# Performance work log

Measured on AMD Instinct MI355X. Metric: run time of the kernel, lower is better.

## Reference

```python
import jax, jax.numpy as jnp
import numpy as np

L, B, S, D, H, DQ, DH = 6, 2, 1024, 1024, 16, 64, 4096  # layers, batch, seq, d_e, heads, d_q, d_h
EPS = 1e-5


def _ln(x, g, b):
    m = jnp.mean(x, axis=-1, keepdims=True)
    v = jnp.mean(jnp.square(x - m), axis=-1, keepdims=True)
    return (x - m) / jnp.sqrt(v + EPS) * g + b


def setup_inputs() -> dict:
    key = jax.random.key(0)
    ks = jax.random.split(key, 8)
    f = lambda k, shape: (jax.random.normal(k, shape, jnp.float32) * 0.02)
    return {
        "x": jax.random.normal(ks[0], (B, S, D), jnp.float32),
        "mask": jnp.zeros((B, S, S), dtype=bool),
        "Wq": f(ks[1], (L, D, H * DQ)), "bq": jnp.zeros((L, H * DQ), jnp.float32),
        "Wk": f(ks[2], (L, D, H * DQ)), "bk": jnp.zeros((L, H * DQ), jnp.float32),
        "Wv": f(ks[3], (L, D, H * DQ)), "bv": jnp.zeros((L, H * DQ), jnp.float32),
        "Wo": f(ks[4], (L, H * DQ, D)), "bo": jnp.zeros((L, D), jnp.float32),
        "ln1_g": jnp.ones((L, D), jnp.float32), "ln1_b": jnp.zeros((L, D), jnp.float32),
        "W1": f(ks[5], (L, D, DH)), "b1": jnp.zeros((L, DH), jnp.float32),
        "W2": f(ks[6], (L, DH, D)), "b2": jnp.zeros((L, D), jnp.float32),
        "ln2_g": jnp.ones((L, D), jnp.float32), "ln2_b": jnp.zeros((L, D), jnp.float32),
    }


def _encoder(x, mask, Wq, bq, Wk, bk, Wv, bv, Wo, bo, ln1_g, ln1_b, W1, b1, W2, b2, ln2_g, ln2_b):
    scale = 1.0 / np.sqrt(DQ).astype(np.float32)

    def step(h, p):
        wq, q_b, wk, k_b, wv, v_b, wo, o_b, g1, be1, w1, f_b1, w2, f_b2, g2, be2 = p
        q = (h @ wq + q_b).reshape(B, S, H, DQ)
        k = (h @ wk + k_b).reshape(B, S, H, DQ)
        v = (h @ wv + v_b).reshape(B, S, H, DQ)
        scores = jnp.einsum('bqhd,bkhd->bhqk', q, k) * scale  # [B,H,S,S]
        scores = jnp.where(mask[:, None, :, :], jnp.float32(-1e9), scores)
        attn = jax.nn.softmax(scores, axis=-1)
        ctx = jnp.einsum('bhqk,bkhd->bqhd', attn, v).reshape(B, S, H * DQ)
        h = _ln(h + ctx @ wo + o_b, g1, be1)
        ff = jax.nn.relu(h @ w1 + f_b1) @ w2 + f_b2  # 1x1 conv1d FFN == pointwise MLP
        h = _ln(h + ff, g2, be2)
        return h, None

    params = (Wq, bq, Wk, bk, Wv, bv, Wo, bo, ln1_g, ln1_b, W1, b1, W2, b2, ln2_g, ln2_b)
    out, _ = jax.lax.scan(step, x, params)
    return out


def reference(x, mask, Wq, bq, Wk, bk, Wv, bv, Wo, bo, ln1_g, ln1_b, W1, b1, W2, b2, ln2_g, ln2_b):
    return _encoder(x, mask, Wq, bq, Wk, bk, Wv, bv, Wo, bo, ln1_g, ln1_b, W1, b1, W2, b2, ln2_g, ln2_b)
```

## Files before the change

### kernel.cpp

```cpp
#include <hip/hip_runtime.h>


typedef unsigned short u16;
typedef __attribute__((ext_vector_type(8))) short bh8;
typedef __attribute__((ext_vector_type(4))) float f32x4;

#define PLANE (2048ull * 1024ull)

__device__ __forceinline__ u16 f2b(float f) {
    unsigned u = __float_as_uint(f);
    u += 0x7fffu + ((u >> 16) & 1u);
    return (u16)(u >> 16);
}
__device__ __forceinline__ void gl_lds16(const void* g, void* l) {
    __builtin_amdgcn_global_load_lds((const __attribute__((address_space(1))) void*)g,
                                     (__attribute__((address_space(3))) void*)l, 16, 0, 0);
}

#define MFMA(a, b, c) __builtin_amdgcn_mfma_f32_16x16x32_bf16((a), (b), (c), 0, 0, 0)

__device__ __forceinline__ void xcd_remap(int nx, int& bx, int& by) {
    int id = blockIdx.y * nx + blockIdx.x;
    int cpx = (nx * gridDim.y) >> 3;
    int sid = (id & 7) * cpx + (id >> 3);
    bx = sid & (nx - 1);
    by = sid / nx;
}

__global__ __launch_bounds__(256) void init_h(const float* __restrict__ x,
                                              u16* __restrict__ hbf, float* __restrict__ hf, int n4) {
    int i = blockIdx.x * 256 + threadIdx.x;
    if (i < n4) {
        float4 v = ((const float4*)x)[i];
        ((float4*)hf)[i] = v;
        u16 t[4] = { f2b(v.x), f2b(v.y), f2b(v.z), f2b(v.w) };
        ((ushort4*)hbf)[i] = *(const ushort4*)t;
    }
}

__device__ __forceinline__ void tp_tile_f2b(const float* __restrict__ in, u16* __restrict__ out,
                                            int R, int C, int ty, int tx) {
    const int r0 = ty * 64, c0 = tx * 64;
    __shared__ alignas(16) float tile[64][68];
    const int tid = threadIdx.x;
#pragma unroll
    for (int it = 0; it < 4; ++it) {
        int s = it * 256 + tid;
        int rr = s >> 4, c4 = (s & 15) * 4;
        float4 v = *(const float4*)&in[(size_t)(r0 + rr) * C + c0 + c4];
        int gsw = ((c4 >> 2) ^ (rr >> 3)) << 2;
        *(float4*)&tile[rr][gsw] = v;
    }
    __syncthreads();
#pragma unroll
    for (int it = 0; it < 2; ++it) {
        int chunk = it * 256 + tid, cc = chunk >> 3, r8 = chunk & 7;
        u16 tmp[8];
#pragma unroll
        for (int j = 0; j < 8; ++j) {
            int r = r8 * 8 + j;
            int col = ((((cc >> 2) ^ (r >> 3)) << 2) | (cc & 3));
            tmp[j] = f2b(tile[r][col]);
        }
        *(uint4*)&out[(size_t)(c0 + cc) * R + r0 + r8 * 8] = *(const uint4*)tmp;
    }
}

__global__ __launch_bounds__(256) void transpose_weights(
        const float* __restrict__ Wq, const float* __restrict__ Wk,
        const float* __restrict__ Wv, const float* __restrict__ Wo,
        const float* __restrict__ W1, const float* __restrict__ W2,
        u16* __restrict__ WT) {
    const int t = blockIdx.x;
    const int l = t / 3072, u = t - l * 3072;
    const size_t M1 = 1024ull * 1024ull;
    const float* wq = Wq + (size_t)l * M1;
    const float* wk = Wk + (size_t)l * M1;
    const float* wv = Wv + (size_t)l * M1;
    const float* wo = Wo + (size_t)l * M1;
    const float* w1 = W1 + (size_t)l * 4 * M1;
    const float* w2 = W2 + (size_t)l * 4 * M1;
    u16* base = WT + (size_t)l * 12 * M1;
    if (u < 1024) {
        int wsel = u >> 8, uu = u & 255;
        const float* src = wsel == 0 ? wq : wsel == 1 ? wk : wsel == 2 ? wv : wo;
        u16* dst = base + (size_t)wsel * M1;
        tp_tile_f2b(src, dst, 1024, 1024, uu >> 4, uu & 15);
    } else if (u < 2048) {
        int uu = u - 1024;
        tp_tile_f2b(w1, base + 4 * M1, 1024, 4096, uu >> 6, uu & 63);
    } else {
        int uu = u - 2048;
        tp_tile_f2b(w2, base + 8 * M1, 4096, 1024, uu >> 4, uu & 15);
    }
}

template<int NB>
__device__ __forceinline__ void stage_ab(const u16* const ap[4], const u16* const bp[NB],
                                         int koff, u16* As, u16* Bs, int tid) {
#pragma unroll
    for (int it = 0; it < 4; ++it) gl_lds16(ap[it] + koff, As + (it * 256 + tid) * 8);
#pragma unroll
    for (int it = 0; it < NB; ++it) gl_lds16(bp[it] + koff, Bs + (it * 256 + tid) * 8);
}

template<int NI>
__device__ __forceinline__ void gemm_compute(const u16* As, const u16* Bs,
                                             int wave, int quad, int l16, f32x4 acc[2][NI]) {
#pragma unroll
    for (int ks = 0; ks < 2; ++ks) {
        bh8 af[2], bf[NI];
#pragma unroll
        for (int mi = 0; mi < 2; ++mi)
            af[mi] = *(const bh8*)&As[(wave * 32 + mi * 16 + l16) * 64 + ((ks * 4 + quad) ^ (l16 & 7)) * 8];
#pragma unroll
        for (int ni = 0; ni < NI; ++ni)
            bf[ni] = *(const bh8*)&Bs[(ni * 16 + l16) * 64 + ((ks * 4 + quad) ^ (l16 & 7)) * 8];
#pragma unroll
        for (int mi = 0; mi < 2; ++mi)
#pragma unroll
            for (int ni = 0; ni < NI; ++ni)
                acc[mi][ni] = MFMA(af[mi], bf[ni], acc[mi][ni]);
    }
}

template<int NI>
__device__ __forceinline__ void gemm_loopT(const u16* __restrict__ A, const u16* __restrict__ BT,
                                           int K, int kb, int ke, int bm, int bn, f32x4 acc[2][NI]) {
    constexpr int NB = NI / 2;
    __shared__ alignas(16) u16 As0[128 * 64];
    __shared__ alignas(16) u16 Bs0[NI * 16 * 64];
    __shared__ alignas(16) u16 As1[128 * 64];
    __shared__ alignas(16) u16 Bs1[NI * 16 * 64];
    const int tid = threadIdx.x;
    const int lane = tid & 63, wave = tid >> 6;
    const int quad = lane >> 4, l16 = lane & 15;

    const u16* ap[4];
    const u16* bp[NB];
#pragma unroll
    for (int it = 0; it < 4; ++it) {
        int chunk = it * 256 + tid, row = chunk >> 3, sseg = (chunk & 7) ^ (row & 7);
        ap[it] = A + (size_t)(bm + row) * K + kb + sseg * 8;
    }
#pragma unroll
    for (int it = 0; it < NB; ++it) {
        int chunk = it * 256 + tid, row = chunk >> 3, sseg = (chunk & 7) ^ (row & 7);
        bp[it] = BT + (size_t)(bn + row) * K + kb + sseg * 8;
    }

    stage_ab<NB>(ap, bp, 0, As0, Bs0, tid);
    __syncthreads();
    for (int k0 = kb; k0 < ke; k0 += 128) {
        stage_ab<NB>(ap, bp, k0 + 64 - kb, As1, Bs1, tid);
        gemm_compute<NI>(As0, Bs0, wave, quad, l16, acc);
        __syncthreads();
        const bool more = (k0 + 128) < ke;
        if (more) stage_ab<NB>(ap, bp, k0 + 128 - kb, As0, Bs0, tid);
        gemm_compute<NI>(As1, Bs1, wave, quad, l16, acc);
        if (more) __syncthreads();
    }
}

__global__ __launch_bounds__(256) void qkv_gemm(const u16* __restrict__ A,
        const u16* __restrict__ BTq, const u16* __restrict__ BTk, const u16* __restrict__ BTv,
        const float* __restrict__ bq, const float* __restrict__ bk, const float* __restrict__ bv,
        u16* __restrict__ Oq, u16* __restrict__ Ok, u16* __restrict__ OvT) {
    int bx, by;
    xcd_remap(16, bx, by);
    const int z = blockIdx.z;
    const u16* BT = z == 0 ? BTq : (z == 1 ? BTk : BTv);
    const float* bias = z == 0 ? bq : (z == 1 ? bk : bv);
    const int bm = by * 128, bn = bx * 64;
    f32x4 acc[2][4] = {};
    gemm_loopT<4>(A, BT, 1024, 0, 1024, bm, bn, acc);

    const int lane = threadIdx.x & 63, wave = threadIdx.x >> 6;
    const int quad = lane >> 4, l16 = lane & 15;
    const float scale = (z == 0) ? 0.125f : 1.0f;
#pragma unroll
    for (int mi = 0; mi < 2; ++mi) {
        int row0 = bm + wave * 32 + mi * 16 + quad * 4;
#pragma unroll
        for (int ni = 0; ni < 4; ++ni) {
            int col = bn + ni * 16 + l16;
            float bv_ = bias[col];
            if (z < 2) {
                u16* O = z == 0 ? Oq : Ok;
#pragma unroll
                for (int r = 0; r < 4; ++r)
                    O[(size_t)(row0 + r) * 1024 + col] = f2b((acc[mi][ni][r] + bv_) * scale);
            } else {
                int b = row0 >> 10, s0 = row0 & 1023;
                u16 tmp[4];
#pragma unroll
                for (int r = 0; r < 4; ++r) tmp[r] = f2b(acc[mi][ni][r] + bv_);
                *(ushort4*)&OvT[(size_t)(b * 1024 + col) * 1024 + s0] = *(const ushort4*)tmp;
            }
        }
    }
}

__global__ __launch_bounds__(256) void gemm_relu(const u16* __restrict__ A, const u16* __restrict__ BT,
        const float* __restrict__ bias, u16* __restrict__ Cb, int N, int K) {
    int bx, by;
    xcd_remap(32, bx, by);
    const int bm = by * 128, bn = bx * 128;
    f32x4 acc[2][8] = {};
    gemm_loopT<8>(A, BT, K, 0, K, bm, bn, acc);
    const int lane = threadIdx.x & 63, wave = threadIdx.x >> 6;
    const int quad = lane >> 4, l16 = lane & 15;
#pragma unroll
    for (int mi = 0; mi < 2; ++mi) {
        int row0 = bm + wave * 32 + mi * 16 + quad * 4;
#pragma unroll
        for (int ni = 0; ni < 8; ++ni) {
            int col = bn + ni * 16 + l16;
            float bv = bias[col];
#pragma unroll
            for (int r = 0; r < 4; ++r)
                Cb[(size_t)(row0 + r) * N + col] = f2b(fmaxf(acc[mi][ni][r] + bv, 0.0f));
        }
    }
}

template<int NI>
__global__ __launch_bounds__(256) void gemm_splitk(const u16* __restrict__ A, const u16* __restrict__ BT,
        float* __restrict__ P, int K, int slice) {
    int bx, by;
    xcd_remap(NI == 8 ? 8 : 16, bx, by);
    const int bm = by * 128, bn = bx * (NI * 16), s = blockIdx.z;
    f32x4 acc[2][NI] = {};
    gemm_loopT<NI>(A, BT, K, s * slice, (s + 1) * slice, bm, bn, acc);
    float* Pl = P + (size_t)s * PLANE;
    const int lane = threadIdx.x & 63, wave = threadIdx.x >> 6;
    const int quad = lane >> 4, l16 = lane & 15;
#pragma unroll
    for (int mi = 0; mi < 2; ++mi) {
        int row0 = bm + wave * 32 + mi * 16 + quad * 4;
#pragma unroll
        for (int ni = 0; ni < NI; ++ni) {
            int col = bn + ni * 16 + l16;
#pragma unroll
            for (int r = 0; r < 4; ++r)
                Pl[(size_t)(row0 + r) * 1024 + col] = acc[mi][ni][r];
        }
    }
}

__device__ __forceinline__ void attn_stageK(const u16* k, int b, int h, int kv0, u16* Ks) {
    const int tid = threadIdx.x;
#pragma unroll
    for (int i = 0; i < 2; ++i) {
        int chunk = i * 256 + tid, rr = chunk >> 3, seg = (chunk & 7) ^ (rr & 7);
        gl_lds16(k + (size_t)(b * 1024 + kv0 + rr) * 1024 + h * 64 + seg * 8, Ks + chunk * 8);
    }
}
__device__ __forceinline__ void attn_stageV(const u16* vT, int bh, int kv0, u16* VTs) {
    const int tid = threadIdx.x;
#pragma unroll
    for (int i = 0; i < 2; ++i) {
        int chunk = i * 256 + tid, rr = chunk >> 3, seg = (chunk & 7) ^ (rr & 7);
        gl_lds16(vT + (size_t)(bh * 64 + rr) * 1024 + kv0 + seg * 8, VTs + chunk * 8);
    }
}

__device__ __forceinline__ void attn_tile(const u16* Qs, const u16* Ksc, const u16* VTsc,
        u16* Ksn, u16* VTsn, u16* Psw, const u16* k, const u16* vT,
        const unsigned char* __restrict__ mask, int b, int h, int bh, int q0, int kv0, bool pre,
        int wave, int quad, int l16, float l[4], f32x4 o[4]) {
    if (pre) attn_stageK(k, b, h, kv0 + 64, Ksn);

    f32x4 st[4] = {};
#pragma unroll
    for (int ks = 0; ks < 2; ++ks) {
        bh8 a = *(const bh8*)&Qs[(wave * 16 + l16) * 64 + ((ks * 4 + quad) ^ (l16 & 7)) * 8];
#pragma unroll
        for (int ni = 0; ni < 4; ++ni) {
            bh8 bb = *(const bh8*)&Ksc[(ni * 16 + l16) * 64 + ((ks * 4 + quad) ^ (l16 & 7)) * 8];
            st[ni] = MFMA(a, bb, st[ni]);
        }
    }

#pragma unroll
    for (int r = 0; r < 4; ++r) {
        int qg = q0 + wave * 16 + quad * 4 + r;
        int prow = quad * 4 + r;
        float p[4], rs = 0.0f;
#pragma unroll
        for (int ni = 0; ni < 4; ++ni) {
            float sv = st[ni][r];
            int kg = kv0 + ni * 16 + l16;
            if (mask[(size_t)b * 1048576 + (size_t)qg * 1024 + kg]) sv = -1e9f;
            p[ni] = __expf(sv);
            rs += p[ni];
        }
#pragma unroll
        for (int off = 1; off < 16; off <<= 1) rs += __shfl_xor(rs, off, 64);
        l[r] += rs;
#pragma unroll
        for (int ni = 0; ni < 4; ++ni) {
            int cchunk = ((ni * 2) + (l16 >> 3)) ^ (prow & 7);
            Psw[prow * 64 + cchunk * 8 + (l16 & 7)] = f2b(p[ni]);
        }
    }
    __syncthreads();
    if (pre) attn_stageV(vT, bh, kv0 + 64, VTsn);

#pragma unroll
    for (int ks = 0; ks < 2; ++ks) {
        bh8 a = *(const bh8*)&Psw[l16 * 64 + ((ks * 4 + quad) ^ (l16 & 7)) * 8];
#pragma unroll
        for (int ni = 0; ni < 4; ++ni) {
            bh8 bb = *(const bh8*)&VTsc[(ni * 16 + l16) * 64 + ((ks * 4 + quad) ^ (l16 & 7)) * 8];
            o[ni] = MFMA(a, bb, o[ni]);
        }
    }
}

__global__ __launch_bounds__(256) void attn_kernel(const u16* __restrict__ q, const u16* __restrict__ k,
        const u16* __restrict__ vT, const unsigned char* __restrict__ mask, u16* __restrict__ ctx) {
    __shared__ alignas(16) u16 Qs[64 * 64];
    __shared__ alignas(16) u16 Ks0[64 * 64];
    __shared__ alignas(16) u16 Ks1[64 * 64];
    __shared__ alignas(16) u16 VTs0[64 * 64];
    __shared__ alignas(16) u16 VTs1[64 * 64];
    __shared__ alignas(16) u16 Ps[4][16 * 64];
    const int tid = threadIdx.x, lane = tid & 63, wave = tid >> 6;
    const int quad = lane >> 4, l16 = lane & 15;
    int bx, by;
    xcd_remap(16, bx, by);
    const int bh = by, b = bh >> 4, h = bh & 15;
    const int q0 = bx * 64;

#pragma unroll
    for (int i = 0; i < 2; ++i) {
        int chunk = i * 256 + tid, rr = chunk >> 3, seg = (chunk & 7) ^ (rr & 7);
        gl_lds16(q + (size_t)(b * 1024 + q0 + rr) * 1024 + h * 64 + seg * 8, Qs + chunk * 8);
    }
    attn_stageK(k, b, h, 0, Ks0);
    attn_stageV(vT, bh, 0, VTs0);
    __syncthreads();

    float l[4] = {0.0f, 0.0f, 0.0f, 0.0f};
    f32x4 o[4] = {};
    for (int kv0 = 0; kv0 < 1024; kv0 += 128) {
        attn_tile(Qs, Ks0, VTs0, Ks1, VTs1, Ps[wave], k, vT, mask, b, h, bh, q0,
                  kv0, true, wave, quad, l16, l, o);
        attn_tile(Qs, Ks1, VTs1, Ks0, VTs0, Ps[wave], k, vT, mask, b, h, bh, q0,
                  kv0 + 64, (kv0 + 128) < 1024, wave, quad, l16, l, o);
    }

#pragma unroll
    for (int r = 0; r < 4; ++r) {
        float inv = 1.0f / l[r];
#pragma unroll
        for (int ni = 0; ni < 4; ++ni) {
            size_t idx = (size_t)(b * 1024 + q0 + wave * 16 + quad * 4 + r) * 1024 + h * 64 + ni * 16 + l16;
            ctx[idx] = f2b(o[ni][r] * inv);
        }
    }
}

__global__ __launch_bounds__(256) void ln_reduce(const float* __restrict__ P, int np,
        const float* __restrict__ bias, const float* __restrict__ res,
        const float* __restrict__ g, const float* __restrict__ bb,
        u16* __restrict__ outb, float* __restrict__ outf) {
    const int row = blockIdx.x, tid = threadIdx.x;
    const int lane = tid & 63, wave = tid >> 6;
    const int c4 = tid * 4;
    const size_t base = (size_t)row * 1024 + c4;
    float4 t = *(const float4*)&res[base];
    float4 bi = *(const float4*)&bias[c4];
    t.x += bi.x; t.y += bi.y; t.z += bi.z; t.w += bi.w;
    for (int p = 0; p < np; ++p) {
        float4 q = *(const float4*)&P[(size_t)p * PLANE + base];
        t.x += q.x; t.y += q.y; t.z += q.z; t.w += q.w;
    }
    float s = t.x + t.y + t.z + t.w;
    float sq = t.x * t.x + t.y * t.y + t.z * t.z + t.w * t.w;
#pragma unroll
    for (int off = 32; off > 0; off >>= 1) { s += __shfl_down(s, off, 64); sq += __shfl_down(sq, off, 64); }
    __shared__ float ps[4], pq[4];
    if (lane == 0) { ps[wave] = s; pq[wave] = sq; }
    __syncthreads();
    s = ps[0] + ps[1] + ps[2] + ps[3];
    sq = pq[0] + pq[1] + pq[2] + pq[3];
    const float mean = s * (1.0f / 1024.0f);
    const float var = sq * (1.0f / 1024.0f) - mean * mean;
    const float rstd = rsqrtf(var + 1e-5f);
    float4 gg = *(const float4*)&g[c4];
    float4 bv = *(const float4*)&bb[c4];
    float y0 = (t.x - mean) * rstd * gg.x + bv.x;
    float y1 = (t.y - mean) * rstd * gg.y + bv.y;
    float y2 = (t.z - mean) * rstd * gg.z + bv.z;
    float y3 = (t.w - mean) * rstd * gg.w + bv.w;
    *(float4*)&outf[base] = make_float4(y0, y1, y2, y3);
    u16 ob[4] = { f2b(y0), f2b(y1), f2b(y2), f2b(y3) };
    *(ushort4*)&outb[base] = *(const ushort4*)ob;
}

extern "C" void kernel_launch(void* const* d_in, const int* in_sizes, int n_in,
                              void* d_out, int out_size, void* d_ws, size_t ws_size,
                              hipStream_t stream) {
    const float* x  = (const float*)d_in[0];
    const unsigned char* mask = (const unsigned char*)d_in[1];
    const float* Wq = (const float*)d_in[2];
    const float* bq = (const float*)d_in[3];
    const float* Wk = (const float*)d_in[4];
    const float* bk = (const float*)d_in[5];
    const float* Wv = (const float*)d_in[6];
    const float* bv = (const float*)d_in[7];
    const float* Wo = (const float*)d_in[8];
    const float* bo = (const float*)d_in[9];
    const float* g1 = (const float*)d_in[10];
    const float* be1= (const float*)d_in[11];
    const float* W1 = (const float*)d_in[12];
    const float* b1 = (const float*)d_in[13];
    const float* W2 = (const float*)d_in[14];
    const float* b2 = (const float*)d_in[15];
    const float* g2 = (const float*)d_in[16];
    const float* be2= (const float*)d_in[17];

    char* w = (char*)d_ws;
    const size_t MB = 1ull << 20;
    if (ws_size < 248 * MB) return;

    float* hf  = (float*)(w + 0 * MB);
    u16*   hbf = (u16*)  (w + 8 * MB);
    u16*   Qb  = (u16*)  (w + 12 * MB);
    u16*   Kb  = (u16*)  (w + 16 * MB);
    u16*   VTb = (u16*)  (w + 24 * MB);
    u16*   CTX = (u16*)  (w + 28 * MB);
    u16*   FF  = (u16*)  (w + 32 * MB);
    float* Pp  = (float*)(w + 72 * MB);
    u16*   WT6 = (u16*)  (w + 104 * MB);

    init_h<<<2048, 256, 0, stream>>>(x, hbf, hf, 512 * 1024);
    transpose_weights<<<18432, 256, 0, stream>>>(Wq, Wk, Wv, Wo, W1, W2, WT6);

    const size_t M1 = 1024ull * 1024ull;
    for (int l = 0; l < 6; ++l) {
        u16* base = WT6 + (size_t)l * 12 * M1;
        u16* WqT = base;
        u16* WkT = base + 1 * M1;
        u16* WvT = base + 2 * M1;
        u16* WoT = base + 3 * M1;
        u16* W1T = base + 4 * M1;
        u16* W2T = base + 8 * M1;

        qkv_gemm<<<dim3(16, 16, 3), 256, 0, stream>>>(hbf, WqT, WkT, WvT,
                bq + l * 1024, bk + l * 1024, bv + l * 1024, Qb, Kb, VTb);
        attn_kernel<<<dim3(16, 32), 256, 0, stream>>>(Qb, Kb, VTb, mask, CTX);
        gemm_splitk<4><<<dim3(16, 16, 2), 256, 0, stream>>>(CTX, WoT, Pp, 1024, 512);
        ln_reduce<<<2048, 256, 0, stream>>>(Pp, 2, bo + l * 1024, hf,
                g1 + l * 1024, be1 + l * 1024, hbf, hf);
        gemm_relu<<<dim3(32, 16), 256, 0, stream>>>(hbf, W1T, b1 + l * 4096, FF, 4096, 1024);
        gemm_splitk<8><<<dim3(8, 16, 4), 256, 0, stream>>>(FF, W2T, Pp, 4096, 1024);
        float* outf = (l == 5) ? (float*)d_out : hf;
        ln_reduce<<<2048, 256, 0, stream>>>(Pp, 4, b2 + l * 1024, hf,
                g2 + l * 1024, be2 + l * 1024, hbf, outf);
    }
}
```

Baseline: 1.131 ms.

## Pipeline weight transpose with async LDS loads and raise MFMA wave priority

The weight transpose kernel now has each block process 8 tiles. Tiles are triple-buffered in LDS and loaded with direct global-to-LDS loads, so the loads overlap with the conversion and stores, and the launch uses far fewer blocks. Separately, s_setprio brackets are placed around the MFMA sections of the GEMM and attention inner loops to favour waves issuing matrix ops. The transpose gains bigger LDS use and manual vmcnt waits, which risk correctness if the wait counts are off.

Measured after the change: 1.338 ms. +18.3%, slower.

```diff
diff --git a/kernel.cpp b/kernel.cpp
--- a/kernel.cpp
+++ b/kernel.cpp
@@ -38,20 +38,44 @@
     }
 }
 
-__device__ __forceinline__ void tp_tile_f2b(const float* __restrict__ in, u16* __restrict__ out,
-                                            int R, int C, int ty, int tx) {
-    const int r0 = ty * 64, c0 = tx * 64;
-    __shared__ alignas(16) float tile[64][68];
-    const int tid = threadIdx.x;
+__device__ __forceinline__ void tw_params(int t,
+        const float* __restrict__ Wq, const float* __restrict__ Wk,
+        const float* __restrict__ Wv, const float* __restrict__ Wo,
+        const float* __restrict__ W1, const float* __restrict__ W2,
+        u16* __restrict__ WT,
+        const float*& src, u16*& dst, int& R, int& C, int& r0, int& c0) {
+    const int l = t / 3072, u = t - l * 3072;
+    const size_t M1 = 1024ull * 1024ull;
+    u16* base = WT + (size_t)l * 12 * M1;
+    if (u < 1024) {
+        int wsel = u >> 8, uu = u & 255;
+        src = (wsel == 0 ? Wq : wsel == 1 ? Wk : wsel == 2 ? Wv : Wo) + (size_t)l * M1;
+        dst = base + (size_t)wsel * M1;
+        R = 1024; C = 1024; r0 = (uu >> 4) * 64; c0 = (uu & 15) * 64;
+    } else if (u < 2048) {
+        int uu = u - 1024;
+        src = W1 + (size_t)l * 4 * M1; dst = base + 4 * M1;
+        R = 1024; C = 4096; r0 = (uu >> 6) * 64; c0 = (uu & 63) * 64;
+    } else {
+        int uu = u - 2048;
+        src = W2 + (size_t)l * 4 * M1; dst = base + 8 * M1;
+        R = 4096; C = 1024; r0 = (uu >> 4) * 64; c0 = (uu & 15) * 64;
+    }
+}
+
+__device__ __forceinline__ void tw_stage(const float* __restrict__ src, int C, int r0, int c0,
+                                         float* buf, int tid) {
 #pragma unroll
     for (int it = 0; it < 4; ++it) {
-        int s = it * 256 + tid;
-        int rr = s >> 4, c4 = (s & 15) * 4;
-        float4 v = *(const float4*)&in[(size_t)(r0 + rr) * C + c0 + c4];
-        int gsw = ((c4 >> 2) ^ (rr >> 3)) << 2;
-        *(float4*)&tile[rr][gsw] = v;
-    }
-    __syncthreads();
+        int chunk = it * 256 + tid;
+        int rr = chunk >> 4, gl = chunk & 15;
+        int gsrc = gl ^ (rr >> 3);
+        gl_lds16(src + (size_t)(r0 + rr) * C + c0 + gsrc * 4, buf + chunk * 4);
+    }
+}
+
+__device__ __forceinline__ void tw_store(u16* __restrict__ dst, int R, int r0, int c0,
+                                         const float* buf, int tid) {
 #pragma unroll
     for (int it = 0; it < 2; ++it) {
         int chunk = it * 256 + tid, cc = chunk >> 3, r8 = chunk & 7;
@@ -60,9 +84,9 @@
         for (int j = 0; j < 8; ++j) {
             int r = r8 * 8 + j;
             int col = ((((cc >> 2) ^ (r >> 3)) << 2) | (cc & 3));
-            tmp[j] = f2b(tile[r][col]);
-        }
-        *(uint4*)&out[(size_t)(c0 + cc) * R + r0 + r8 * 8] = *(const uint4*)tmp;
+            tmp[j] = f2b(buf[r * 64 + col]);
+        }
+        *(uint4*)&dst[(size_t)(c0 + cc) * R + r0 + r8 * 8] = *(const uint4*)tmp;
     }
 }
 
@@ -71,27 +95,25 @@
         const float* __restrict__ Wv, const float* __restrict__ Wo,
         const float* __restrict__ W1, const float* __restrict__ W2,
         u16* __restrict__ WT) {
-    const int t = blockIdx.x;
-    const int l = t / 3072, u = t - l * 3072;
-    const size_t M1 = 1024ull * 1024ull;
-    const float* wq = Wq + (size_t)l * M1;
-    const float* wk = Wk + (size_t)l * M1;
-    const float* wv = Wv + (size_t)l * M1;
-    const float* wo = Wo + (size_t)l * M1;
-    const float* w1 = W1 + (size_t)l * 4 * M1;
-    const float* w2 = W2 + (size_t)l * 4 * M1;
-    u16* base = WT + (size_t)l * 12 * M1;
-    if (u < 1024) {
-        int wsel = u >> 8, uu = u & 255;
-        const float* src = wsel == 0 ? wq : wsel == 1 ? wk : wsel == 2 ? wv : wo;
-        u16* dst = base + (size_t)wsel * M1;
-        tp_tile_f2b(src, dst, 1024, 1024, uu >> 4, uu & 15);
-    } else if (u < 2048) {
-        int uu = u - 1024;
-        tp_tile_f2b(w1, base + 4 * M1, 1024, 4096, uu >> 6, uu & 63);
-    } else {
-        int uu = u - 2048;
-        tp_tile_f2b(w2, base + 8 * M1, 4096, 1024, uu >> 4, uu & 15);
+    __shared__ alignas(16) float buf[3][64 * 64];
+    const int tid = threadIdx.x;
+    const int t0 = blockIdx.x * 8;
+
+    const float* src[8]; u16* dst[8]; int R[8], C[8], r0[8], c0[8];
+#pragma unroll
+    for (int i = 0; i < 8; ++i)
+        tw_params(t0 + i, Wq, Wk, Wv, Wo, W1, W2, WT, src[i], dst[i], R[i], C[i], r0[i], c0[i]);
+
+    tw_stage(src[0], C[0], r0[0], c0[0], buf[0], tid);
+    tw_stage(src[1], C[1], r0[1], c0[1], buf[1], tid);
+#pragma unroll
+    for (int i = 0; i < 8; ++i) {
+        if (i + 1 < 8) asm volatile("s_waitcnt vmcnt(4)" ::: "memory");
+        else           asm volatile("s_waitcnt vmcnt(0)" ::: "memory");
+        __builtin_amdgcn_s_barrier();
+        __builtin_amdgcn_sched_barrier(0);
+        if (i + 2 < 8) tw_stage(src[i + 2], C[i + 2], r0[i + 2], c0[i + 2], buf[(i + 2) % 3], tid);
+        tw_store(dst[i], R[i], r0[i], c0[i], buf[i % 3], tid);
     }
 }
 
@@ -116,11 +138,13 @@
 #pragma unroll
         for (int ni = 0; ni < NI; ++ni)
             bf[ni] = *(const bh8*)&Bs[(ni * 16 + l16) * 64 + ((ks * 4 + quad) ^ (l16 & 7)) * 8];
+        __builtin_amdgcn_s_setprio(1);
 #pragma unroll
         for (int mi = 0; mi < 2; ++mi)
 #pragma unroll
             for (int ni = 0; ni < NI; ++ni)
                 acc[mi][ni] = MFMA(af[mi], bf[ni], acc[mi][ni]);
+        __builtin_amdgcn_s_setprio(0);
     }
 }
 
@@ -272,6 +296,7 @@
     if (pre) attn_stageK(k, b, h, kv0 + 64, Ksn);
 
     f32x4 st[4] = {};
+    __builtin_amdgcn_s_setprio(1);
 #pragma unroll
     for (int ks = 0; ks < 2; ++ks) {
         bh8 a = *(const bh8*)&Qs[(wave * 16 + l16) * 64 + ((ks * 4 + quad) ^ (l16 & 7)) * 8];
@@ -281,6 +306,7 @@
             st[ni] = MFMA(a, bb, st[ni]);
         }
     }
+    __builtin_amdgcn_s_setprio(0);
 
 #pragma unroll
     for (int r = 0; r < 4; ++r) {
@@ -307,6 +333,7 @@
     __syncthreads();
     if (pre) attn_stageV(vT, bh, kv0 + 64, VTsn);
 
+    __builtin_amdgcn_s_setprio(1);
 #pragma unroll
     for (int ks = 0; ks < 2; ++ks) {
         bh8 a = *(const bh8*)&Psw[l16 * 64 + ((ks * 4 + quad) ^ (l16 & 7)) * 8];
@@ -316,6 +343,7 @@
             o[ni] = MFMA(a, bb, o[ni]);
         }
     }
+    __builtin_amdgcn_s_setprio(0);
 }
 
 __global__ __launch_bounds__(256) void attn_kernel(const u16* __restrict__ q, const u16* __restrict__ k,
@@ -437,7 +465,7 @@
     u16*   WT6 = (u16*)  (w + 104 * MB);
 
     init_h<<<2048, 256, 0, stream>>>(x, hbf, hf, 512 * 1024);
-    transpose_weights<<<18432, 256, 0, stream>>>(Wq, Wk, Wv, Wo, W1, W2, WT6);
+    transpose_weights<<<2304, 256, 0, stream>>>(Wq, Wk, Wv, Wo, W1, W2, WT6);
 
     const size_t M1 = 1024ull * 1024ull;
     for (int l = 0; l < 6; ++l) {
```
